# Optimization experiments

Hardware: AMD Instinct MI355X
Metric: run time of the kernel (lower is better)

## Reference

```python
import jax, jax.numpy as jnp
import numpy as np

N = 8192        # nodes
E = 262144      # edges (avg degree 32)
D = 128         # input_dim
H = 128         # hidden_dim
O = 64          # output_dim (classes)
C = 4096        # codebook_size
LAMB_EDGE = 1.0
LAMB_NODE = 1.0
COMMIT_W = 0.25


def l2norm(x):
    return x / jnp.clip(jnp.linalg.norm(x, axis=-1, keepdims=True), 1e-12)


def graph_conv(x, W, b, src, dst, n):
    # DGL GraphConv, norm='both': D_out^{-1/2} on src, sum-aggregate, D_in^{-1/2} on dst, then xW+b, relu
    ones = jnp.ones(src.shape[0], x.dtype)
    deg_out = jax.ops.segment_sum(ones, src, num_segments=n)
    deg_in = jax.ops.segment_sum(ones, dst, num_segments=n)
    norm_src = jnp.where(deg_out > 0, jax.lax.rsqrt(jnp.maximum(deg_out, 1e-12)), 0.0)
    norm_dst = jnp.where(deg_in > 0, jax.lax.rsqrt(jnp.maximum(deg_in, 1e-12)), 0.0)
    h = x * norm_src[:, None]
    m = jax.ops.segment_sum(h[src], dst, num_segments=n)  # message passing (irregular gather/scatter)
    h = m * norm_dst[:, None]
    return jax.nn.relu(h @ W + b)


def setup_inputs() -> dict:
    key = jax.random.key(0)
    ks = jax.random.split(key, 16)
    feats = jax.random.normal(ks[0], (N, D), jnp.float32)
    src = jax.random.randint(ks[1], (E,), 0, N)
    dst = jax.random.randint(ks[2], (E,), 0, N)
    s = 1.0 / np.sqrt(D)
    sh = 1.0 / np.sqrt(H)
    return {
        'feats': feats, 'src': src, 'dst': dst,
        'W1': jax.random.normal(ks[3], (D, D), jnp.float32) * s,
        'b1': jnp.zeros((D,), jnp.float32),
        'W2': jax.random.normal(ks[4], (D, H), jnp.float32) * s,
        'b2': jnp.zeros((H,), jnp.float32),
        'dec1_W': jax.random.normal(ks[5], (D, D), jnp.float32) * s,
        'dec1_b': jnp.zeros((D,), jnp.float32),
        'dec2_W': jax.random.normal(ks[6], (D, D), jnp.float32) * s,
        'dec2_b': jnp.zeros((D,), jnp.float32),
        'lin_W': jax.random.normal(ks[7], (H, O), jnp.float32) * sh,
        'lin_b': jnp.zeros((O,), jnp.float32),
        'codebook': jax.random.normal(ks[8], (C, D), jnp.float32),
    }


def reference(feats, src, dst, W1, b1, W2, b2, dec1_W, dec1_b, dec2_W, dec2_b, lin_W, lin_b, codebook):
    n = feats.shape[0]
    # layer 1: GraphConv(D -> D)
    h1 = graph_conv(feats, W1, b1, src, dst, n)  # [N, D]

    # VectorQuantize with cosine similarity codebook
    xn = l2norm(h1)
    cn = l2norm(codebook)                 # [C, D]
    dist = xn @ cn.T                      # [N, C] cosine similarity
    ind = jnp.argmax(dist, axis=-1)       # [N]
    q = cn[ind]                           # [N, D] nearest (normalized) codes
    commit_loss = COMMIT_W * jnp.mean((jax.lax.stop_gradient(q) - h1) ** 2)
    quantized = h1 + jax.lax.stop_gradient(q - h1)  # straight-through

    quantized_edge = quantized @ dec1_W + dec1_b
    quantized_node = quantized @ dec2_W + dec2_b
    feature_rec_loss = LAMB_NODE * jnp.mean((h1 - quantized_node) ** 2)

    # dense adjacency reconstruction
    adj = jnp.zeros((n, n), feats.dtype).at[src, dst].set(1.0)
    adj_q = quantized_edge @ quantized_edge.T          # [N, N]
    adj_q = (adj_q - adj_q.min()) / (adj_q.max() - adj_q.min())
    edge_rec_loss = LAMB_EDGE * jnp.sqrt(jnp.mean((adj - adj_q) ** 2))

    # layer 2: GraphConv(D -> H) on quantized_edge, then linear head
    h3 = graph_conv(quantized_edge, W2, b2, src, dst, n)
    out = h3 @ lin_W + lin_b                           # [N, O]

    loss = feature_rec_loss + edge_rec_loss + commit_loss
    h_list = (h1, quantized, h3)
    return (h_list, out, loss, dist, cn)
```

## Files before the change

kernel.cpp:

```cpp
#include <hip/hip_runtime.h>
#include <cstdint>

constexpr int N = 8192, E = 262144, D = 128, O = 64, C = 4096;

#define DEV __device__ __forceinline__

typedef short s8v __attribute__((ext_vector_type(8)));
typedef float f4v __attribute__((ext_vector_type(4)));

DEV unsigned fmap(float f) {
  unsigned u = __float_as_uint(f);
  return (u & 0x80000000u) ? ~u : (u | 0x80000000u);
}
DEV float funmap(unsigned u) {
  unsigned o = (u & 0x80000000u) ? (u & 0x7FFFFFFFu) : ~u;
  return __uint_as_float(o);
}
DEV unsigned short f2bf(float f) {
  uint32_t b = __float_as_uint(f);
  return (unsigned short)((b + 0x7FFFu + ((b >> 16) & 1u)) >> 16);
}
DEV float bf2f(unsigned short h) { return __uint_as_float((uint32_t)h << 16); }


__global__ __launch_bounds__(256) void k_degree(const int* __restrict__ src, const int* __restrict__ dst,
    uint32_t* __restrict__ bits, int* __restrict__ dego, int* __restrict__ degi,
    uint32_t* __restrict__ scal_u) {
  int e = blockIdx.x * 256 + threadIdx.x;
  int s = src[e], d = dst[e];
  atomicAdd(&dego[s], 1);
  atomicAdd(&degi[d], 1);
  unsigned idx = (unsigned)s * 8192u + (unsigned)d;
  unsigned bit = 1u << (idx & 31);
  unsigned old = atomicOr(&bits[idx >> 5], bit);
  bool isnew = !(old & bit);
  unsigned long long b = __ballot(isnew);
  if ((threadIdx.x & 63) == 0) atomicAdd(&scal_u[2], (unsigned)__popcll(b));
}

__global__ __launch_bounds__(256) void k_norms(const int* __restrict__ dego, const int* __restrict__ degi,
                                               float* __restrict__ nsrc, float* __restrict__ ndst) {
  int i = blockIdx.x * 256 + threadIdx.x;
  if (i >= N) return;
  int a = dego[i], b = degi[i];
  nsrc[i] = a > 0 ? 1.0f / sqrtf((float)a) : 0.0f;
  ndst[i] = b > 0 ? 1.0f / sqrtf((float)b) : 0.0f;
}

__global__ __launch_bounds__(1024) void k_scan(const int* __restrict__ degi, int* __restrict__ rowptr,
                                               int* __restrict__ cursor) {
  __shared__ int sh[1024];
  int tid = threadIdx.x;
  int base = tid * 8;
  int v[8];
  int s = 0;
#pragma unroll
  for (int j = 0; j < 8; ++j) { v[j] = degi[base + j]; s += v[j]; }
  sh[tid] = s;
  __syncthreads();
  for (int off = 1; off < 1024; off <<= 1) {
    int t = (tid >= off) ? sh[tid - off] : 0;
    __syncthreads();
    sh[tid] += t;
    __syncthreads();
  }
  int run = (tid == 0) ? 0 : sh[tid - 1];
#pragma unroll
  for (int j = 0; j < 8; ++j) { rowptr[base + j] = run; cursor[base + j] = run; run += v[j]; }
  if (tid == 1023) rowptr[N] = run;
}

__global__ __launch_bounds__(256) void k_scatter(const int* __restrict__ src, const int* __restrict__ dst,
                                                 int* __restrict__ cursor, int* __restrict__ csr) {
  int e = blockIdx.x * 256 + threadIdx.x;
  int d = dst[e];
  int pos = atomicAdd(&cursor[d], 1);
  csr[pos] = src[e];
}

__global__ __launch_bounds__(256) void k_scale(const float4* __restrict__ in, const float* __restrict__ norm,
                                               float4* __restrict__ out) {
  int i = blockIdx.x * 256 + threadIdx.x;
  if (i >= N * 32) return;
  float s = norm[i >> 5];
  float4 v = in[i];
  v.x *= s; v.y *= s; v.z *= s; v.w *= s;
  out[i] = v;
}

__global__ __launch_bounds__(256) void k_tobf16(const float4* __restrict__ in, ushort4* __restrict__ out) {
  int i = blockIdx.x * 256 + threadIdx.x;
  if (i >= N * 32) return;
  float4 v = in[i];
  ushort4 o;
  o.x = f2bf(v.x); o.y = f2bf(v.y); o.z = f2bf(v.z); o.w = f2bf(v.w);
  out[i] = o;
}

__global__ __launch_bounds__(256) void k_split(const float4* __restrict__ in,
    ushort4* __restrict__ hi, ushort4* __restrict__ lo, int n4) {
  int i = blockIdx.x * 256 + threadIdx.x;
  if (i >= n4) return;
  float4 v = in[i];
  ushort4 h, l;
  h.x = f2bf(v.x); h.y = f2bf(v.y); h.z = f2bf(v.z); h.w = f2bf(v.w);
  l.x = f2bf(v.x - bf2f(h.x)); l.y = f2bf(v.y - bf2f(h.y));
  l.z = f2bf(v.z - bf2f(h.z)); l.w = f2bf(v.w - bf2f(h.w));
  hi[i] = h; lo[i] = l;
}

__global__ __launch_bounds__(256) void k_transpose(const float* __restrict__ in, float* __restrict__ outT) {
  __shared__ float tl[64][133];
  int t = threadIdx.x;
  int cbase = blockIdx.x * 64;
#pragma unroll
  for (int it = 0; it < 32; ++it) {
    int idx = t + it * 256;
    int r = idx >> 7, k = idx & 127;
    tl[r][k] = in[(cbase + r) * 128 + k];
  }
  __syncthreads();
#pragma unroll
  for (int it = 0; it < 32; ++it) {
    int idx = t + it * 256;
    int k = idx >> 6, c = idx & 63;
    outT[k * 4096 + cbase + c] = tl[c][k];
  }
}

__global__ __launch_bounds__(128) void k_aggregate(const int* __restrict__ rowptr, const int* __restrict__ csr,
    const float* __restrict__ tmp, const float* __restrict__ ndst, float* __restrict__ out) {
  int row = blockIdx.x, t = threadIdx.x;
  int e0 = rowptr[row], e1 = rowptr[row + 1];
  float acc = 0.f;
  int e = e0;
  for (; e + 4 <= e1; e += 4) {
    int s0 = csr[e], s1 = csr[e + 1], s2 = csr[e + 2], s3 = csr[e + 3];
    acc += tmp[s0 * 128 + t];
    acc += tmp[s1 * 128 + t];
    acc += tmp[s2 * 128 + t];
    acc += tmp[s3 * 128 + t];
  }
  for (; e < e1; ++e) acc += tmp[csr[e] * 128 + t];
  out[row * 128 + t] = acc * ndst[row];
}

__global__ __launch_bounds__(256) void k_l2norm(const float* __restrict__ in, float* __restrict__ out_al,
                                                float* __restrict__ out_extra, int rows) {
  int wave = threadIdx.x >> 6, lane = threadIdx.x & 63;
  int row = blockIdx.x * 4 + wave;
  if (row >= rows) return;
  float2 v = ((const float2*)in)[row * 64 + lane];
  float ss = v.x * v.x + v.y * v.y;
#pragma unroll
  for (int o = 32; o > 0; o >>= 1) ss += __shfl_xor(ss, o);
  float den = fmaxf(sqrtf(ss), 1e-12f);
  float ox = v.x / den, oy = v.y / den;
  ((float2*)out_al)[row * 64 + lane] = make_float2(ox, oy);
  if (out_extra != nullptr) {
    out_extra[row * 128 + 2 * lane] = ox;
    out_extra[row * 128 + 2 * lane + 1] = oy;
  }
}

template <int CO, bool RELU>
__global__ __launch_bounds__(256, 2) void k_mm(const float* __restrict__ A, const float* __restrict__ W,
    const float* __restrict__ bias, float* __restrict__ out) {
  constexpr int CG = CO / 4;
  constexpr int RG = 256 / CG;
  constexpr int TR = RG * 4;
  constexpr int WIT = (64 * CG) / 256;
  __shared__ __align__(16) float Al[TR * 128];
  __shared__ __align__(16) float Wl[64 * CO];
  int tid = threadIdx.x;
  int cg = tid % CG, rg = tid / CG;
  int rbase = blockIdx.x * TR;
#pragma unroll
  for (int it = 0; it < TR / 8; ++it) {
    int idx = tid + it * 256;
    int r = idx >> 5, c = idx & 31;
    *(float4*)&Al[r * 128 + c * 4] = *(const float4*)&A[(rbase + r) * 128 + c * 4];
  }
  float acc[4][4] = {};
  for (int kc = 0; kc < 128; kc += 64) {
    __syncthreads();
#pragma unroll
    for (int it = 0; it < WIT; ++it) {
      int idx = tid + it * 256;
      int r = idx / CG, c = idx % CG;
      *(float4*)&Wl[r * CO + c * 4] = *(const float4*)&W[(kc + r) * CO + c * 4];
    }
    __syncthreads();
#pragma unroll
    for (int k = 0; k < 64; ++k) {
      float4 w4 = *(const float4*)&Wl[k * CO + cg * 4];
#pragma unroll
      for (int i = 0; i < 4; ++i) {
        float a = Al[(rg * 4 + i) * 128 + kc + k];
        acc[i][0] += a * w4.x; acc[i][1] += a * w4.y; acc[i][2] += a * w4.z; acc[i][3] += a * w4.w;
      }
    }
  }
  float4 b4 = *(const float4*)&bias[cg * 4];
#pragma unroll
  for (int i = 0; i < 4; ++i) {
    float4 o;
    o.x = acc[i][0] + b4.x; o.y = acc[i][1] + b4.y; o.z = acc[i][2] + b4.z; o.w = acc[i][3] + b4.w;
    if (RELU) { o.x = fmaxf(o.x, 0.f); o.y = fmaxf(o.y, 0.f); o.z = fmaxf(o.z, 0.f); o.w = fmaxf(o.w, 0.f); }
    *(float4*)&out[(rbase + rg * 4 + i) * CO + cg * 4] = o;
  }
}

__global__ __launch_bounds__(256) void k_dist(
    const unsigned short* __restrict__ xhi, const unsigned short* __restrict__ xlo,
    const unsigned short* __restrict__ chi, const unsigned short* __restrict__ clo,
    float* __restrict__ dout, unsigned long long* __restrict__ pbk, float* __restrict__ pbv2) {
  int bx = blockIdx.x, by = blockIdx.y;
  int rbase = by * 128, cbase = bx * 128;
  __shared__ __align__(16) unsigned short As[128 * 132];
  __shared__ __align__(16) unsigned short Bs[128 * 132];
  int tid = threadIdx.x;
  int wave = tid >> 6, lane = tid & 63;
  int l15 = lane & 15, quad = lane >> 4;
  int wr = wave * 32;

#pragma unroll
  for (int it = 0; it < 8; ++it) {
    int idx = tid + it * 256;
    int r = idx >> 4, ch = idx & 15;
    *(s8v*)&As[r * 132 + ch * 8] = *(const s8v*)&xhi[(rbase + r) * 128 + ch * 8];
    *(s8v*)&Bs[r * 132 + ch * 8] = *(const s8v*)&chi[(cbase + r) * 128 + ch * 8];
  }
  __syncthreads();
  s8v ah[2][4], al[2][4];
#pragma unroll
  for (int rt = 0; rt < 2; ++rt)
#pragma unroll
    for (int kq = 0; kq < 4; ++kq)
      ah[rt][kq] = *(const s8v*)&As[(wr + rt * 16 + l15) * 132 + kq * 32 + quad * 8];
  __syncthreads();
#pragma unroll
  for (int it = 0; it < 8; ++it) {
    int idx = tid + it * 256;
    int r = idx >> 4, ch = idx & 15;
    *(s8v*)&As[r * 132 + ch * 8] = *(const s8v*)&xlo[(rbase + r) * 128 + ch * 8];
  }
  __syncthreads();
#pragma unroll
  for (int rt = 0; rt < 2; ++rt)
#pragma unroll
    for (int kq = 0; kq < 4; ++kq)
      al[rt][kq] = *(const s8v*)&As[(wr + rt * 16 + l15) * 132 + kq * 32 + quad * 8];

  f4v acc[2][8];
#pragma unroll
  for (int rt = 0; rt < 2; ++rt)
#pragma unroll
    for (int ct = 0; ct < 8; ++ct) acc[rt][ct] = {0.f, 0.f, 0.f, 0.f};

#pragma unroll
  for (int ct = 0; ct < 8; ++ct) {
    s8v b[4];
#pragma unroll
    for (int kq = 0; kq < 4; ++kq)
      b[kq] = *(const s8v*)&Bs[(ct * 16 + l15) * 132 + kq * 32 + quad * 8];
#pragma unroll
    for (int rt = 0; rt < 2; ++rt)
#pragma unroll
      for (int kq = 0; kq < 4; ++kq) {
        acc[rt][ct] = __builtin_amdgcn_mfma_f32_16x16x32_bf16(ah[rt][kq], b[kq], acc[rt][ct], 0, 0, 0);
        acc[rt][ct] = __builtin_amdgcn_mfma_f32_16x16x32_bf16(al[rt][kq], b[kq], acc[rt][ct], 0, 0, 0);
      }
  }
  __syncthreads();
#pragma unroll
  for (int it = 0; it < 8; ++it) {
    int idx = tid + it * 256;
    int r = idx >> 4, ch = idx & 15;
    *(s8v*)&Bs[r * 132 + ch * 8] = *(const s8v*)&clo[(cbase + r) * 128 + ch * 8];
  }
  __syncthreads();
#pragma unroll
  for (int ct = 0; ct < 8; ++ct) {
    s8v b[4];
#pragma unroll
    for (int kq = 0; kq < 4; ++kq)
      b[kq] = *(const s8v*)&Bs[(ct * 16 + l15) * 132 + kq * 32 + quad * 8];
#pragma unroll
    for (int rt = 0; rt < 2; ++rt)
#pragma unroll
      for (int kq = 0; kq < 4; ++kq)
        acc[rt][ct] = __builtin_amdgcn_mfma_f32_16x16x32_bf16(ah[rt][kq], b[kq], acc[rt][ct], 0, 0, 0);
  }

  float b1v[2][4], b2v[2][4];
  unsigned c1v[2][4];
#pragma unroll
  for (int rt = 0; rt < 2; ++rt)
#pragma unroll
    for (int reg = 0; reg < 4; ++reg) { b1v[rt][reg] = -3.4e38f; b2v[rt][reg] = -3.4e38f; c1v[rt][reg] = 0; }
#pragma unroll
  for (int rt = 0; rt < 2; ++rt)
#pragma unroll
    for (int ct = 0; ct < 8; ++ct)
#pragma unroll
      for (int reg = 0; reg < 4; ++reg) {
        float v = acc[rt][ct][reg];
        int row = rbase + wr + rt * 16 + quad * 4 + reg;
        int col = cbase + ct * 16 + l15;
        dout[(size_t)row * 4096 + col] = v;
        if (v > b1v[rt][reg]) { b2v[rt][reg] = b1v[rt][reg]; b1v[rt][reg] = v; c1v[rt][reg] = (unsigned)col; }
        else if (v > b2v[rt][reg]) b2v[rt][reg] = v;
      }
  __syncthreads();
  unsigned long long* sck = (unsigned long long*)As;
  float* scv = (float*)Bs;
#pragma unroll
  for (int rt = 0; rt < 2; ++rt)
#pragma unroll
    for (int reg = 0; reg < 4; ++reg) {
      int rloc = wr + rt * 16 + quad * 4 + reg;
      sck[rloc * 16 + l15] =
          (((unsigned long long)fmap(b1v[rt][reg])) << 32) |
          (unsigned long long)(0xFFFFFFFFu - c1v[rt][reg]);
      scv[rloc * 16 + l15] = b2v[rt][reg];
    }
  __syncthreads();
  if (tid < 128) {
    unsigned long long m = 0ull;
#pragma unroll
    for (int l = 0; l < 16; ++l) {
      unsigned long long t = sck[tid * 16 + l];
      m = t > m ? t : m;
    }
    float v2 = -3.4e38f;
#pragma unroll
    for (int l = 0; l < 16; ++l) {
      unsigned long long k = sck[tid * 16 + l];
      float c = (k == m) ? scv[tid * 16 + l] : funmap((unsigned)(k >> 32));
      v2 = fmaxf(v2, c);
    }
    pbk[(size_t)(rbase + tid) * 32 + bx] = m;
    pbv2[(size_t)(rbase + tid) * 32 + bx] = v2;
  }
}

__global__ __launch_bounds__(128) void k_q(const unsigned long long* __restrict__ pbk,
    const float* __restrict__ pbv2, const float* __restrict__ cnws,
    const float* __restrict__ h1, float* __restrict__ qout, float* __restrict__ pq,
    uint32_t* __restrict__ scal_u, int* __restrict__ flagged) {
  int row = blockIdx.x, t = threadIdx.x;
  int e = t & 31;
  unsigned long long k = pbk[(size_t)row * 32 + e];
  float v2l = pbv2[(size_t)row * 32 + e];
  unsigned long long m = k;
#pragma unroll
  for (int o = 32; o > 0; o >>= 1) {
    unsigned long long s = __shfl_xor(m, o);
    m = s > m ? s : m;
  }
  float cand = (k == m) ? v2l : funmap((unsigned)(k >> 32));
#pragma unroll
  for (int o = 32; o > 0; o >>= 1) cand = fmaxf(cand, __shfl_xor(cand, o));
  float gap = funmap((unsigned)(m >> 32)) - cand;
  if (gap < 2e-4f && t == 0) {
    unsigned idx = atomicAdd(&scal_u[3], 1u);
    flagged[idx] = row;
  }
  int col = (int)(0xFFFFFFFFu - (unsigned)(m & 0xFFFFFFFFull));
  float q = cnws[col * 128 + t];
  qout[row * 128 + t] = q;
  float dd = q - h1[row * 128 + t];
  float ss = dd * dd;
#pragma unroll
  for (int o = 32; o > 0; o >>= 1) ss += __shfl_xor(ss, o);
  __shared__ float p[2];
  if ((t & 63) == 0) p[t >> 6] = ss;
  __syncthreads();
  if (t == 0) pq[row] = p[0] + p[1];
}

__global__ __launch_bounds__(256) void k_fix(const uint32_t* __restrict__ scal_u,
    const int* __restrict__ flagged, const float* __restrict__ xn,
    const float* __restrict__ cnwsT, const float* __restrict__ cnws,
    const float* __restrict__ h1, float* __restrict__ qout, float* __restrict__ pq) {
  int nf = (int)scal_u[3];
  int t = threadIdx.x;
  __shared__ float xr[128];
  __shared__ unsigned long long bw4[4];
  __shared__ float pp[2];
  for (int i = blockIdx.x; i < nf; i += gridDim.x) {
    int row = flagged[i];
    __syncthreads();
    if (t < 128) xr[t] = xn[row * 128 + t];
    __syncthreads();
    float s[16];
#pragma unroll
    for (int j = 0; j < 16; ++j) s[j] = 0.f;
    for (int k = 0; k < 128; ++k) {
      float xv = xr[k];
      const float* cp = &cnwsT[k * 4096 + t];
#pragma unroll
      for (int j = 0; j < 16; ++j) s[j] = fmaf(xv, cp[j * 256], s[j]);
    }
    unsigned long long best = 0ull;
#pragma unroll
    for (int j = 0; j < 16; ++j) {
      unsigned c = (unsigned)(j * 256 + t);
      unsigned long long key = (((unsigned long long)fmap(s[j])) << 32) |
                               (unsigned long long)(0xFFFFFFFFu - c);
      if (key > best) best = key;
    }
#pragma unroll
    for (int o = 32; o > 0; o >>= 1) {
      unsigned long long s2 = __shfl_xor(best, o);
      best = s2 > best ? s2 : best;
    }
    if ((t & 63) == 0) bw4[t >> 6] = best;
    __syncthreads();
    unsigned long long b0 = bw4[0] > bw4[1] ? bw4[0] : bw4[1];
    unsigned long long b1 = bw4[2] > bw4[3] ? bw4[2] : bw4[3];
    best = b0 > b1 ? b0 : b1;
    int col = (int)(0xFFFFFFFFu - (unsigned)(best & 0xFFFFFFFFull));
    if (t < 128) {
      float q = cnws[col * 128 + t];
      qout[(size_t)row * 128 + t] = q;
      float dd = q - h1[row * 128 + t];
      float ss = dd * dd;
#pragma unroll
      for (int o = 32; o > 0; o >>= 1) ss += __shfl_xor(ss, o);
      if ((t & 63) == 0) pp[t >> 6] = ss;
    }
    __syncthreads();
    if (t == 0) pq[row] = pp[0] + pp[1];
  }
}

__global__ __launch_bounds__(256) void k_adjq(const unsigned short* __restrict__ qb,
    const uint32_t* __restrict__ bits,
    double* __restrict__ p_sum, double* __restrict__ p_sq, double* __restrict__ p_es,
    float* __restrict__ p_mn, float* __restrict__ p_mx) {
  int bx = blockIdx.x, by = blockIdx.y;
  int pid = by * gridDim.x + bx;
  int tid = threadIdx.x;
  if (bx < by) {
    if (tid == 0) {
      p_sum[pid] = 0.0; p_sq[pid] = 0.0; p_es[pid] = 0.0;
      p_mn[pid] = 3.4e38f; p_mx[pid] = -3.4e38f;
    }
    return;
  }
  int rbase = by * 128, cbase = bx * 128;
  __shared__ unsigned short Ab[128 * 132];
  __shared__ unsigned short Bb[128 * 132];
#pragma unroll
  for (int it = 0; it < 8; ++it) {
    int idx = tid + it * 256;
    int r = idx >> 4, ch = idx & 15;
    *(s8v*)&Ab[r * 132 + ch * 8] = *(const s8v*)&qb[(rbase + r) * 128 + ch * 8];
    *(s8v*)&Bb[r * 132 + ch * 8] = *(const s8v*)&qb[(cbase + r) * 128 + ch * 8];
  }
  __syncthreads();
  int wave = tid >> 6, lane = tid & 63;
  int l15 = lane & 15, quad = lane >> 4;
  int wr = wave * 32;
  f4v acc[2][8];
#pragma unroll
  for (int rt = 0; rt < 2; ++rt)
#pragma unroll
    for (int ct = 0; ct < 8; ++ct) acc[rt][ct] = {0.f, 0.f, 0.f, 0.f};
  s8v a[2][4];
#pragma unroll
  for (int rt = 0; rt < 2; ++rt)
#pragma unroll
    for (int kq = 0; kq < 4; ++kq)
      a[rt][kq] = *(const s8v*)&Ab[(wr + rt * 16 + l15) * 132 + kq * 32 + quad * 8];
#pragma unroll
  for (int ct = 0; ct < 8; ++ct) {
    s8v b[4];
#pragma unroll
    for (int kq = 0; kq < 4; ++kq)
      b[kq] = *(const s8v*)&Bb[(ct * 16 + l15) * 132 + kq * 32 + quad * 8];
#pragma unroll
    for (int rt = 0; rt < 2; ++rt)
#pragma unroll
      for (int kq = 0; kq < 4; ++kq)
        acc[rt][ct] = __builtin_amdgcn_mfma_f32_16x16x32_bf16(a[rt][kq], b[kq], acc[rt][ct], 0, 0, 0);
  }
  __syncthreads();
  uint32_t* bl = (uint32_t*)Ab;
  uint32_t* blT = bl + 512;
#pragma unroll
  for (int it = 0; it < 2; ++it) {
    int idx = tid + it * 256;
    int r = idx >> 2, wq = idx & 3;
    bl[idx] = bits[(rbase + r) * 256 + (cbase >> 5) + wq];
    blT[idx] = bits[(cbase + r) * 256 + (rbase >> 5) + wq];
  }
  __syncthreads();
  float lsum = 0.f, lsq = 0.f, les = 0.f;
  float lmin = 3.4e38f, lmax = -3.4e38f;
  bool diag = (bx == by);
#pragma unroll
  for (int rt = 0; rt < 2; ++rt)
#pragma unroll
    for (int ct = 0; ct < 8; ++ct)
#pragma unroll
      for (int reg = 0; reg < 4; ++reg) {
        int lr = wr + rt * 16 + quad * 4 + reg;
        int lc = ct * 16 + l15;
        if (diag && lc < lr) continue;
        float v = acc[rt][ct][reg];
        bool ondiag = diag && (lc == lr);
        float wgt = ondiag ? 1.f : 2.f;
        lsum += wgt * v;
        lsq += wgt * v * v;
        lmin = fminf(lmin, v);
        lmax = fmaxf(lmax, v);
        unsigned eb = (bl[lr * 4 + (lc >> 5)] >> (lc & 31)) & 1u;
        if (!ondiag) eb += (blT[lc * 4 + (lr >> 5)] >> (lr & 31)) & 1u;
        if (eb) les += (float)eb * v;
      }
  double dsum = (double)lsum, dsq = (double)lsq, des = (double)les;
#pragma unroll
  for (int o = 32; o > 0; o >>= 1) {
    dsum += __shfl_xor(dsum, o);
    dsq += __shfl_xor(dsq, o);
    des += __shfl_xor(des, o);
    lmin = fminf(lmin, __shfl_xor(lmin, o));
    lmax = fmaxf(lmax, __shfl_xor(lmax, o));
  }
  double* shd = (double*)Bb;
  float* shf = (float*)(shd + 12);
  if (lane == 0) {
    shd[wave * 3 + 0] = dsum; shd[wave * 3 + 1] = dsq; shd[wave * 3 + 2] = des;
    shf[wave * 2 + 0] = lmin; shf[wave * 2 + 1] = lmax;
  }
  __syncthreads();
  if (tid == 0) {
    double s = 0.0, q = 0.0, e = 0.0;
    float m0 = 3.4e38f, m1 = -3.4e38f;
#pragma unroll
    for (int w0 = 0; w0 < 4; ++w0) {
      s += shd[w0 * 3 + 0]; q += shd[w0 * 3 + 1]; e += shd[w0 * 3 + 2];
      m0 = fminf(m0, shf[w0 * 2 + 0]); m1 = fmaxf(m1, shf[w0 * 2 + 1]);
    }
    p_sum[pid] = s; p_sq[pid] = q; p_es[pid] = e;
    p_mn[pid] = m0; p_mx[pid] = m1;
  }
}

__global__ __launch_bounds__(256) void k_sqdiff(const float4* __restrict__ a, const float4* __restrict__ b,
                                                float* __restrict__ ps) {
  int i = blockIdx.x * 256 + threadIdx.x;
  float s = 0.f;
  const int total = N * 32;
  for (; i < total; i += gridDim.x * 256) {
    float4 x = a[i], y = b[i];
    float d0 = x.x - y.x, d1 = x.y - y.y, d2 = x.z - y.z, d3 = x.w - y.w;
    s += d0 * d0 + d1 * d1 + d2 * d2 + d3 * d3;
  }
#pragma unroll
  for (int o = 32; o > 0; o >>= 1) s += __shfl_xor(s, o);
  __shared__ float p[4];
  if ((threadIdx.x & 63) == 0) p[threadIdx.x >> 6] = s;
  __syncthreads();
  if (threadIdx.x == 0) ps[blockIdx.x] = p[0] + p[1] + p[2] + p[3];
}

__global__ __launch_bounds__(1024) void k_finish(const double* __restrict__ p_sum,
    const double* __restrict__ p_sq, const double* __restrict__ p_es,
    const float* __restrict__ p_mn, const float* __restrict__ p_mx,
    const float* __restrict__ pq, const float* __restrict__ ps,
    const uint32_t* __restrict__ scal_u, float* __restrict__ o_loss) {
  int tid = threadIdx.x;
  double sum = 0.0, sq = 0.0, es = 0.0, commit = 0.0, frec = 0.0;
  float mn = 3.4e38f, mx = -3.4e38f;
  for (int i = tid; i < 4096; i += 1024) {
    sum += p_sum[i]; sq += p_sq[i]; es += p_es[i];
    mn = fminf(mn, p_mn[i]); mx = fmaxf(mx, p_mx[i]);
  }
  for (int i = tid; i < 8192; i += 1024) commit += (double)pq[i];
  if (tid < 512) frec = (double)ps[tid];
#pragma unroll
  for (int o = 32; o > 0; o >>= 1) {
    sum += __shfl_xor(sum, o); sq += __shfl_xor(sq, o); es += __shfl_xor(es, o);
    commit += __shfl_xor(commit, o); frec += __shfl_xor(frec, o);
    mn = fminf(mn, __shfl_xor(mn, o)); mx = fmaxf(mx, __shfl_xor(mx, o));
  }
  __shared__ double shd[16][5];
  __shared__ float shf[16][2];
  int wave = tid >> 6, lane = tid & 63;
  if (lane == 0) {
    shd[wave][0] = sum; shd[wave][1] = sq; shd[wave][2] = es;
    shd[wave][3] = commit; shd[wave][4] = frec;
    shf[wave][0] = mn; shf[wave][1] = mx;
  }
  __syncthreads();
  if (tid == 0) {
    double s = 0, q = 0, e = 0, c = 0, f = 0;
    float m0 = 3.4e38f, m1 = -3.4e38f;
    for (int w0 = 0; w0 < 16; ++w0) {
      s += shd[w0][0]; q += shd[w0][1]; e += shd[w0][2]; c += shd[w0][3]; f += shd[w0][4];
      m0 = fminf(m0, shf[w0][0]); m1 = fmaxf(m1, shf[w0][1]);
    }
    double mnd = (double)m0, mxd = (double)m1, U = (double)scal_u[2];
    const double N2 = 67108864.0;
    double scl = 1.0 / (mxd - mnd);
    double mean = (scl * scl * (q - 2.0 * mnd * s + mnd * mnd * N2) - 2.0 * scl * (e - mnd * U) + U) / N2;
    *o_loss = (float)(f / 1048576.0 + sqrt(mean) + 0.25 * c / 1048576.0);
  }
}

extern "C" void kernel_launch(void* const* d_in, const int* in_sizes, int n_in,
                              void* d_out, int out_size, void* d_ws, size_t ws_size,
                              hipStream_t stream) {
  (void)in_sizes; (void)n_in; (void)out_size;
  const float* feats = (const float*)d_in[0];
  const int* src = (const int*)d_in[1];
  const int* dst = (const int*)d_in[2];
  const float* W1 = (const float*)d_in[3];
  const float* b1 = (const float*)d_in[4];
  const float* W2 = (const float*)d_in[5];
  const float* b2 = (const float*)d_in[6];
  const float* dec1W = (const float*)d_in[7];
  const float* dec1b = (const float*)d_in[8];
  const float* dec2W = (const float*)d_in[9];
  const float* dec2b = (const float*)d_in[10];
  const float* linW = (const float*)d_in[11];
  const float* linb = (const float*)d_in[12];
  const float* codebook = (const float*)d_in[13];

  float* out = (float*)d_out;
  float* o_h1 = out;
  float* o_q = out + 1048576;
  float* o_h3 = out + 2097152;
  float* o_out = out + 3145728;
  float* o_loss = out + 3670016;
  float* o_dist = out + 3670017;
  float* o_cn = out + 37224449;

  char* w = (char*)d_ws;
  size_t off = 0;
  auto alloc = [&](size_t b) { char* p = w + off; off = (off + b + 255) & ~(size_t)255; return p; };
  uint32_t* bits = (uint32_t*)alloc(8388608);
  int* dego = (int*)alloc(N * 4);
  int* degi = (int*)alloc(N * 4);
  uint32_t* scal_u = (uint32_t*)alloc(256);
  size_t zero_bytes = off;
  int* rowptr = (int*)alloc((N + 1) * 4);
  int* cursor = (int*)alloc(N * 4);
  int* csr = (int*)alloc(E * 4);
  float* nsrc = (float*)alloc(N * 4);
  float* ndst = (float*)alloc(N * 4);
  float* tmp = (float*)alloc((size_t)N * D * 4);
  float* agg = (float*)alloc((size_t)N * D * 4);
  float* xn = (float*)alloc((size_t)N * D * 4);
  float* cnws = (float*)alloc((size_t)C * D * 4);
  float* qe = (float*)alloc((size_t)N * D * 4);
  float* qn = (float*)alloc((size_t)N * D * 4);
  double* p_sum = (double*)alloc(4096 * 8);
  double* p_sq = (double*)alloc(4096 * 8);
  double* p_es = (double*)alloc(4096 * 8);
  float* p_mn = (float*)alloc(4096 * 4);
  float* p_mx = (float*)alloc(4096 * 4);
  float* pq = (float*)alloc(8192 * 4);
  float* ps = (float*)alloc(512 * 4);
  int* flagged = (int*)alloc(8192 * 4);
  unsigned short* qb = (unsigned short*)tmp;
  float* cnwsT = tmp;
  unsigned short* xhi = (unsigned short*)qe;
  unsigned short* xlo = (unsigned short*)(qe + 524288);
  unsigned short* chi = (unsigned short*)qn;
  unsigned short* clo = (unsigned short*)(qn + 262144);
  unsigned long long* pbk = (unsigned long long*)agg;
  float* pbv2 = (float*)(agg + 524288);
  if (ws_size < off) return;

  hipMemsetAsync(d_ws, 0, zero_bytes, stream);

  k_degree<<<E / 256, 256, 0, stream>>>(src, dst, bits, dego, degi, scal_u);
  k_norms<<<N / 256, 256, 0, stream>>>(dego, degi, nsrc, ndst);
  k_scan<<<1, 1024, 0, stream>>>(degi, rowptr, cursor);
  k_scatter<<<E / 256, 256, 0, stream>>>(src, dst, cursor, csr);

  k_scale<<<N * 32 / 256, 256, 0, stream>>>((const float4*)feats, nsrc, (float4*)tmp);
  k_aggregate<<<N, 128, 0, stream>>>(rowptr, csr, tmp, ndst, agg);
  k_mm<128, true><<<N / 32, 256, 0, stream>>>(agg, W1, b1, o_h1);

  k_l2norm<<<C / 4, 256, 0, stream>>>(codebook, cnws, o_cn, C);
  k_l2norm<<<N / 4, 256, 0, stream>>>(o_h1, xn, nullptr, N);
  k_transpose<<<C / 64, 256, 0, stream>>>(cnws, cnwsT);
  k_split<<<N * 32 / 256, 256, 0, stream>>>((const float4*)xn, (ushort4*)xhi, (ushort4*)xlo, N * 32);
  k_split<<<C * 32 / 256, 256, 0, stream>>>((const float4*)cnws, (ushort4*)chi, (ushort4*)clo, C * 32);
  k_dist<<<dim3(C / 128, N / 128), 256, 0, stream>>>(xhi, xlo, chi, clo, o_dist, pbk, pbv2);
  k_q<<<N, 128, 0, stream>>>(pbk, pbv2, cnws, o_h1, o_q, pq, scal_u, flagged);
  k_fix<<<128, 256, 0, stream>>>(scal_u, flagged, xn, cnwsT, cnws, o_h1, o_q, pq);

  k_mm<128, false><<<N / 32, 256, 0, stream>>>(o_q, dec1W, dec1b, qe);
  k_mm<128, false><<<N / 32, 256, 0, stream>>>(o_q, dec2W, dec2b, qn);
  k_sqdiff<<<512, 256, 0, stream>>>((const float4*)o_h1, (const float4*)qn, ps);

  k_tobf16<<<N * 32 / 256, 256, 0, stream>>>((const float4*)qe, (ushort4*)qb);
  k_adjq<<<dim3(N / 128, N / 128), 256, 0, stream>>>(qb, bits, p_sum, p_sq, p_es, p_mn, p_mx);

  k_scale<<<N * 32 / 256, 256, 0, stream>>>((const float4*)qe, nsrc, (float4*)tmp);
  k_aggregate<<<N, 128, 0, stream>>>(rowptr, csr, tmp, ndst, agg);
  k_mm<128, true><<<N / 32, 256, 0, stream>>>(agg, W2, b2, o_h3);
  k_mm<64, false><<<N / 64, 256, 0, stream>>>(o_h3, linW, linb, o_out);

  k_finish<<<1, 1024, 0, stream>>>(p_sum, p_sq, p_es, p_mn, p_mx, pq, ps, scal_u, o_loss);
}
```

Before: 526.7 us.

## Fuse elementwise kernels into neighbors and merge decoder matmuls with loss

Folds the degree-norm computation into the scan kernel, folds the source-norm scaling into the CSR aggregation, folds the bf16 hi/lo split into the l2norm kernel, and fuses both decoder matmuls, the bf16 conversion and the feature reconstruction squared-diff into one kernel. This removes several small launches and full-array round trips through global memory (scaled copies, qn, split buffers). In exchange the aggregation does an extra gather of nsrc per edge, and the fused decoder kernel uses more shared memory and registers.

```diff
diff --git a/kernel.cpp b/kernel.cpp
--- a/kernel.cpp
+++ b/kernel.cpp
@@ -38,24 +38,22 @@
   if ((threadIdx.x & 63) == 0) atomicAdd(&scal_u[2], (unsigned)__popcll(b));
 }
 
-__global__ __launch_bounds__(256) void k_norms(const int* __restrict__ dego, const int* __restrict__ degi,
-                                               float* __restrict__ nsrc, float* __restrict__ ndst) {
-  int i = blockIdx.x * 256 + threadIdx.x;
-  if (i >= N) return;
-  int a = dego[i], b = degi[i];
-  nsrc[i] = a > 0 ? 1.0f / sqrtf((float)a) : 0.0f;
-  ndst[i] = b > 0 ? 1.0f / sqrtf((float)b) : 0.0f;
-}
-
-__global__ __launch_bounds__(1024) void k_scan(const int* __restrict__ degi, int* __restrict__ rowptr,
-                                               int* __restrict__ cursor) {
+__global__ __launch_bounds__(1024) void k_scan(const int* __restrict__ degi, const int* __restrict__ dego,
+    int* __restrict__ rowptr, int* __restrict__ cursor,
+    float* __restrict__ nsrc, float* __restrict__ ndst) {
   __shared__ int sh[1024];
   int tid = threadIdx.x;
   int base = tid * 8;
   int v[8];
   int s = 0;
 #pragma unroll
-  for (int j = 0; j < 8; ++j) { v[j] = degi[base + j]; s += v[j]; }
+  for (int j = 0; j < 8; ++j) {
+    v[j] = degi[base + j];
+    int a = dego[base + j];
+    nsrc[base + j] = a > 0 ? 1.0f / sqrtf((float)a) : 0.0f;
+    ndst[base + j] = v[j] > 0 ? 1.0f / sqrtf((float)v[j]) : 0.0f;
+    s += v[j];
+  }
   sh[tid] = s;
   __syncthreads();
   for (int off = 1; off < 1024; off <<= 1) {
@@ -78,75 +76,27 @@
   csr[pos] = src[e];
 }
 
-__global__ __launch_bounds__(256) void k_scale(const float4* __restrict__ in, const float* __restrict__ norm,
-                                               float4* __restrict__ out) {
-  int i = blockIdx.x * 256 + threadIdx.x;
-  if (i >= N * 32) return;
-  float s = norm[i >> 5];
-  float4 v = in[i];
-  v.x *= s; v.y *= s; v.z *= s; v.w *= s;
-  out[i] = v;
-}
-
-__global__ __launch_bounds__(256) void k_tobf16(const float4* __restrict__ in, ushort4* __restrict__ out) {
-  int i = blockIdx.x * 256 + threadIdx.x;
-  if (i >= N * 32) return;
-  float4 v = in[i];
-  ushort4 o;
-  o.x = f2bf(v.x); o.y = f2bf(v.y); o.z = f2bf(v.z); o.w = f2bf(v.w);
-  out[i] = o;
-}
-
-__global__ __launch_bounds__(256) void k_split(const float4* __restrict__ in,
-    ushort4* __restrict__ hi, ushort4* __restrict__ lo, int n4) {
-  int i = blockIdx.x * 256 + threadIdx.x;
-  if (i >= n4) return;
-  float4 v = in[i];
-  ushort4 h, l;
-  h.x = f2bf(v.x); h.y = f2bf(v.y); h.z = f2bf(v.z); h.w = f2bf(v.w);
-  l.x = f2bf(v.x - bf2f(h.x)); l.y = f2bf(v.y - bf2f(h.y));
-  l.z = f2bf(v.z - bf2f(h.z)); l.w = f2bf(v.w - bf2f(h.w));
-  hi[i] = h; lo[i] = l;
-}
-
-__global__ __launch_bounds__(256) void k_transpose(const float* __restrict__ in, float* __restrict__ outT) {
-  __shared__ float tl[64][133];
-  int t = threadIdx.x;
-  int cbase = blockIdx.x * 64;
-#pragma unroll
-  for (int it = 0; it < 32; ++it) {
-    int idx = t + it * 256;
-    int r = idx >> 7, k = idx & 127;
-    tl[r][k] = in[(cbase + r) * 128 + k];
-  }
-  __syncthreads();
-#pragma unroll
-  for (int it = 0; it < 32; ++it) {
-    int idx = t + it * 256;
-    int k = idx >> 6, c = idx & 63;
-    outT[k * 4096 + cbase + c] = tl[c][k];
-  }
-}
-
-__global__ __launch_bounds__(128) void k_aggregate(const int* __restrict__ rowptr, const int* __restrict__ csr,
-    const float* __restrict__ tmp, const float* __restrict__ ndst, float* __restrict__ out) {
+__global__ __launch_bounds__(128) void k_aggscale(const int* __restrict__ rowptr, const int* __restrict__ csr,
+    const float* __restrict__ x, const float* __restrict__ nsrc, const float* __restrict__ ndst,
+    float* __restrict__ out) {
   int row = blockIdx.x, t = threadIdx.x;
   int e0 = rowptr[row], e1 = rowptr[row + 1];
   float acc = 0.f;
   int e = e0;
   for (; e + 4 <= e1; e += 4) {
     int s0 = csr[e], s1 = csr[e + 1], s2 = csr[e + 2], s3 = csr[e + 3];
-    acc += tmp[s0 * 128 + t];
-    acc += tmp[s1 * 128 + t];
-    acc += tmp[s2 * 128 + t];
-    acc += tmp[s3 * 128 + t];
-  }
-  for (; e < e1; ++e) acc += tmp[csr[e] * 128 + t];
-  out[row * 128 + t] = acc * ndst[row];
-}
-
-__global__ __launch_bounds__(256) void k_l2norm(const float* __restrict__ in, float* __restrict__ out_al,
-                                                float* __restrict__ out_extra, int rows) {
+    float n0 = nsrc[s0], n1 = nsrc[s1], n2 = nsrc[s2], n3 = nsrc[s3];
+    acc = __fadd_rn(acc, __fmul_rn(x[s0 * 128 + t], n0));
+    acc = __fadd_rn(acc, __fmul_rn(x[s1 * 128 + t], n1));
+    acc = __fadd_rn(acc, __fmul_rn(x[s2 * 128 + t], n2));
+    acc = __fadd_rn(acc, __fmul_rn(x[s3 * 128 + t], n3));
+  }
+  for (; e < e1; ++e) acc = __fadd_rn(acc, __fmul_rn(x[csr[e] * 128 + t], nsrc[csr[e]]));
+  out[row * 128 + t] = __fmul_rn(acc, ndst[row]);
+}
+
+__global__ __launch_bounds__(256) void k_l2ns(const float* __restrict__ in, float* __restrict__ out_al,
+    float* __restrict__ out_extra, ushort2* __restrict__ hi, ushort2* __restrict__ lo, int rows) {
   int wave = threadIdx.x >> 6, lane = threadIdx.x & 63;
   int row = blockIdx.x * 4 + wave;
   if (row >= rows) return;
@@ -160,6 +110,30 @@
   if (out_extra != nullptr) {
     out_extra[row * 128 + 2 * lane] = ox;
     out_extra[row * 128 + 2 * lane + 1] = oy;
+  }
+  ushort2 h, l;
+  h.x = f2bf(ox); h.y = f2bf(oy);
+  l.x = f2bf(ox - bf2f(h.x)); l.y = f2bf(oy - bf2f(h.y));
+  hi[row * 64 + lane] = h;
+  lo[row * 64 + lane] = l;
+}
+
+__global__ __launch_bounds__(256) void k_transpose(const float* __restrict__ in, float* __restrict__ outT) {
+  __shared__ float tl[64][133];
+  int t = threadIdx.x;
+  int cbase = blockIdx.x * 64;
+#pragma unroll
+  for (int it = 0; it < 32; ++it) {
+    int idx = t + it * 256;
+    int r = idx >> 7, k = idx & 127;
+    tl[r][k] = in[(cbase + r) * 128 + k];
+  }
+  __syncthreads();
+#pragma unroll
+  for (int it = 0; it < 32; ++it) {
+    int idx = t + it * 256;
+    int k = idx >> 6, c = idx & 63;
+    outT[k * 4096 + cbase + c] = tl[c][k];
   }
 }
 
@@ -209,6 +183,75 @@
     if (RELU) { o.x = fmaxf(o.x, 0.f); o.y = fmaxf(o.y, 0.f); o.z = fmaxf(o.z, 0.f); o.w = fmaxf(o.w, 0.f); }
     *(float4*)&out[(rbase + rg * 4 + i) * CO + cg * 4] = o;
   }
+}
+
+__global__ __launch_bounds__(256, 3) void k_dec(const float* __restrict__ A,
+    const float* __restrict__ W1, const float* __restrict__ b1,
+    const float* __restrict__ W2, const float* __restrict__ b2,
+    const float* __restrict__ h1, float* __restrict__ qe, unsigned short* __restrict__ qb,
+    float* __restrict__ ps) {
+  __shared__ __align__(16) float Al[32 * 128];
+  __shared__ __align__(16) float Wl1[32 * 128];
+  __shared__ __align__(16) float Wl2[32 * 128];
+  int tid = threadIdx.x;
+  int cg = tid & 31, rg = tid >> 5;
+  int rbase = blockIdx.x * 32;
+#pragma unroll
+  for (int it = 0; it < 4; ++it) {
+    int idx = tid + it * 256;
+    int r = idx >> 5, c = idx & 31;
+    *(float4*)&Al[r * 128 + c * 4] = *(const float4*)&A[(rbase + r) * 128 + c * 4];
+  }
+  float acc1[4][4] = {}, acc2[4][4] = {};
+  for (int kc = 0; kc < 128; kc += 32) {
+    __syncthreads();
+#pragma unroll
+    for (int it = 0; it < 4; ++it) {
+      int idx = tid + it * 256;
+      int r = idx >> 5, c = idx & 31;
+      *(float4*)&Wl1[r * 128 + c * 4] = *(const float4*)&W1[(kc + r) * 128 + c * 4];
+      *(float4*)&Wl2[r * 128 + c * 4] = *(const float4*)&W2[(kc + r) * 128 + c * 4];
+    }
+    __syncthreads();
+#pragma unroll
+    for (int k = 0; k < 32; ++k) {
+      float4 w1 = *(const float4*)&Wl1[k * 128 + cg * 4];
+      float4 w2 = *(const float4*)&Wl2[k * 128 + cg * 4];
+#pragma unroll
+      for (int i = 0; i < 4; ++i) {
+        float a = Al[(rg * 4 + i) * 128 + kc + k];
+        acc1[i][0] += a * w1.x; acc1[i][1] += a * w1.y; acc1[i][2] += a * w1.z; acc1[i][3] += a * w1.w;
+        acc2[i][0] += a * w2.x; acc2[i][1] += a * w2.y; acc2[i][2] += a * w2.z; acc2[i][3] += a * w2.w;
+      }
+    }
+  }
+  float4 bb1 = *(const float4*)&b1[cg * 4];
+  float4 bb2 = *(const float4*)&b2[cg * 4];
+  float s = 0.f;
+#pragma unroll
+  for (int i = 0; i < 4; ++i) {
+    int row = rbase + rg * 4 + i;
+    float4 o;
+    o.x = acc1[i][0] + bb1.x; o.y = acc1[i][1] + bb1.y;
+    o.z = acc1[i][2] + bb1.z; o.w = acc1[i][3] + bb1.w;
+    *(float4*)&qe[row * 128 + cg * 4] = o;
+    ushort4 ob;
+    ob.x = f2bf(o.x); ob.y = f2bf(o.y); ob.z = f2bf(o.z); ob.w = f2bf(o.w);
+    *(ushort4*)&qb[row * 128 + cg * 4] = ob;
+    float4 h = *(const float4*)&h1[row * 128 + cg * 4];
+    float d0 = acc2[i][0] + bb2.x - h.x;
+    float d1 = acc2[i][1] + bb2.y - h.y;
+    float d2 = acc2[i][2] + bb2.z - h.z;
+    float d3 = acc2[i][3] + bb2.w - h.w;
+    s += d0 * d0 + d1 * d1 + d2 * d2 + d3 * d3;
+  }
+#pragma unroll
+  for (int o = 32; o > 0; o >>= 1) s += __shfl_xor(s, o);
+  __syncthreads();
+  float* shp = Al;
+  if ((tid & 63) == 0) shp[tid >> 6] = s;
+  __syncthreads();
+  if (tid == 0) ps[blockIdx.x] = shp[0] + shp[1] + shp[2] + shp[3];
 }
 
 __global__ __launch_bounds__(256) void k_dist(
@@ -550,24 +593,6 @@
   }
 }
 
-__global__ __launch_bounds__(256) void k_sqdiff(const float4* __restrict__ a, const float4* __restrict__ b,
-                                                float* __restrict__ ps) {
-  int i = blockIdx.x * 256 + threadIdx.x;
-  float s = 0.f;
-  const int total = N * 32;
-  for (; i < total; i += gridDim.x * 256) {
-    float4 x = a[i], y = b[i];
-    float d0 = x.x - y.x, d1 = x.y - y.y, d2 = x.z - y.z, d3 = x.w - y.w;
-    s += d0 * d0 + d1 * d1 + d2 * d2 + d3 * d3;
-  }
-#pragma unroll
-  for (int o = 32; o > 0; o >>= 1) s += __shfl_xor(s, o);
-  __shared__ float p[4];
-  if ((threadIdx.x & 63) == 0) p[threadIdx.x >> 6] = s;
-  __syncthreads();
-  if (threadIdx.x == 0) ps[blockIdx.x] = p[0] + p[1] + p[2] + p[3];
-}
-
 __global__ __launch_bounds__(1024) void k_finish(const double* __restrict__ p_sum,
     const double* __restrict__ p_sq, const double* __restrict__ p_es,
     const float* __restrict__ p_mn, const float* __restrict__ p_mx,
@@ -581,7 +606,7 @@
     mn = fminf(mn, p_mn[i]); mx = fmaxf(mx, p_mx[i]);
   }
   for (int i = tid; i < 8192; i += 1024) commit += (double)pq[i];
-  if (tid < 512) frec = (double)ps[tid];
+  if (tid < 256) frec = (double)ps[tid];
 #pragma unroll
   for (int o = 32; o > 0; o >>= 1) {
     sum += __shfl_xor(sum, o); sq += __shfl_xor(sq, o); es += __shfl_xor(es, o);
@@ -680,32 +705,24 @@
   hipMemsetAsync(d_ws, 0, zero_bytes, stream);
 
   k_degree<<<E / 256, 256, 0, stream>>>(src, dst, bits, dego, degi, scal_u);
-  k_norms<<<N / 256, 256, 0, stream>>>(dego, degi, nsrc, ndst);
-  k_scan<<<1, 1024, 0, stream>>>(degi, rowptr, cursor);
+  k_scan<<<1, 1024, 0, stream>>>(degi, dego, rowptr, cursor, nsrc, ndst);
   k_scatter<<<E / 256, 256, 0, stream>>>(src, dst, cursor, csr);
 
-  k_scale<<<N * 32 / 256, 256, 0, stream>>>((const float4*)feats, nsrc, (float4*)tmp);
-  k_aggregate<<<N, 128, 0, stream>>>(rowptr, csr, tmp, ndst, agg);
+  k_aggscale<<<N, 128, 0, stream>>>(rowptr, csr, feats, nsrc, ndst, agg);
   k_mm<128, true><<<N / 32, 256, 0, stream>>>(agg, W1, b1, o_h1);
 
-  k_l2norm<<<C / 4, 256, 0, stream>>>(codebook, cnws, o_cn, C);
-  k_l2norm<<<N / 4, 256, 0, stream>>>(o_h1, xn, nullptr, N);
+  k_l2ns<<<C / 4, 256, 0, stream>>>(codebook, cnws, o_cn, (ushort2*)chi, (ushort2*)clo, C);
+  k_l2ns<<<N / 4, 256, 0, stream>>>(o_h1, xn, nullptr, (ushort2*)xhi, (ushort2*)xlo, N);
   k_transpose<<<C / 64, 256, 0, stream>>>(cnws, cnwsT);
-  k_split<<<N * 32 / 256, 256, 0, stream>>>((const float4*)xn, (ushort4*)xhi, (ushort4*)xlo, N * 32);
-  k_split<<<C * 32 / 256, 256, 0, stream>>>((const float4*)cnws, (ushort4*)chi, (ushort4*)clo, C * 32);
   k_dist<<<dim3(C / 128, N / 128), 256, 0, stream>>>(xhi, xlo, chi, clo, o_dist, pbk, pbv2);
   k_q<<<N, 128, 0, stream>>>(pbk, pbv2, cnws, o_h1, o_q, pq, scal_u, flagged);
   k_fix<<<128, 256, 0, stream>>>(scal_u, flagged, xn, cnwsT, cnws, o_h1, o_q, pq);
 
-  k_mm<128, false><<<N / 32, 256, 0, stream>>>(o_q, dec1W, dec1b, qe);
-  k_mm<128, false><<<N / 32, 256, 0, stream>>>(o_q, dec2W, dec2b, qn);
-  k_sqdiff<<<512, 256, 0, stream>>>((const float4*)o_h1, (const float4*)qn, ps);
-
-  k_tobf16<<<N * 32 / 256, 256, 0, stream>>>((const float4*)qe, (ushort4*)qb);
+  k_dec<<<N / 32, 256, 0, stream>>>(o_q, dec1W, dec1b, dec2W, dec2b, o_h1, qe, qb, ps);
+
   k_adjq<<<dim3(N / 128, N / 128), 256, 0, stream>>>(qb, bits, p_sum, p_sq, p_es, p_mn, p_mx);
 
-  k_scale<<<N * 32 / 256, 256, 0, stream>>>((const float4*)qe, nsrc, (float4*)tmp);
-  k_aggregate<<<N, 128, 0, stream>>>(rowptr, csr, tmp, ndst, agg);
+  k_aggscale<<<N, 128, 0, stream>>>(rowptr, csr, qe, nsrc, ndst, agg);
   k_mm<128, true><<<N / 32, 256, 0, stream>>>(agg, W2, b2, o_h3);
   k_mm<64, false><<<N / 64, 256, 0, stream>>>(o_h3, linW, linb, o_out);
 
```

After: 521.3 us. No clear change (-1.0%).
